# Kernel tuning notes

Measured on AMD Instinct MI355X. Metric: run time of the kernel, lower is better.

The kernel has to match this reference:

```python
import jax, jax.numpy as jnp
import numpy as np

N_NODES = 100000
N_EDGES = 3200000
N_FEAT = 64
HIDDEN = 20
N_CLASSES = 10
BN_EPS = 1e-5


def _lin_init(key, fan_in, fan_out):
    k1, k2 = jax.random.split(key)
    bound = 1.0 / np.sqrt(fan_in)
    W = jax.random.uniform(k1, (fan_in, fan_out), jnp.float32, -bound, bound)
    b = jax.random.uniform(k2, (fan_out,), jnp.float32, -bound, bound)
    return W, b


def setup_inputs() -> dict:
    key = jax.random.key(0)
    ks = jax.random.split(key, 12)
    x = jax.random.normal(ks[0], (N_NODES, N_FEAT), jnp.float32)
    edge_index = jax.random.randint(ks[1], (2, N_EDGES), 0, N_NODES, jnp.int32)
    edge_weights = jax.random.uniform(ks[2], (N_EDGES,), jnp.float32)
    w1a, b1a = _lin_init(ks[3], N_FEAT, HIDDEN)
    w2a, b2a = _lin_init(ks[4], HIDDEN, HIDDEN)
    w1b, b1b = _lin_init(ks[5], HIDDEN, HIDDEN)
    w2b, b2b = _lin_init(ks[6], HIDDEN, HIDDEN)
    w1c, b1c = _lin_init(ks[7], HIDDEN, HIDDEN)
    w2c, b2c = _lin_init(ks[8], HIDDEN, HIDDEN)
    wlin, blin = _lin_init(ks[9], 3 * HIDDEN, N_CLASSES)
    g1 = jnp.ones((HIDDEN,), jnp.float32); be1 = jnp.zeros((HIDDEN,), jnp.float32)
    g2 = jnp.ones((HIDDEN,), jnp.float32); be2 = jnp.zeros((HIDDEN,), jnp.float32)
    return {
        'x': x, 'edge_index': edge_index, 'edge_weights': edge_weights,
        'w1a': w1a, 'b1a': b1a, 'w2a': w2a, 'b2a': b2a, 'g1': g1, 'be1': be1,
        'w1b': w1b, 'b1b': b1b, 'w2b': w2b, 'b2b': b2b, 'g2': g2, 'be2': be2,
        'w1c': w1c, 'b1c': b1c, 'w2c': w2c, 'b2c': b2c,
        'wlin': wlin, 'blin': blin,
    }


def _gin_conv(h, src, dst, w, W1, b1, W2, b2):
    # gather source node features, scale per-edge, scatter-add at destination
    m = h[src] * w[:, None]                                  # [E, d]
    agg = jax.ops.segment_sum(m, dst, num_segments=N_NODES)  # [N, d]
    z = jax.nn.relu(agg @ W1 + b1)
    return jax.nn.relu(z @ W2 + b2)


def _bn(h, gamma, beta):
    mu = jnp.mean(h, axis=0)
    var = jnp.var(h, axis=0)
    return gamma * (h - mu) * jax.lax.rsqrt(var + BN_EPS) + beta


def reference(x, edge_index, edge_weights,
              w1a, b1a, w2a, b2a, g1, be1,
              w1b, b1b, w2b, b2b, g2, be2,
              w1c, b1c, w2c, b2c, wlin, blin):
    src, dst = edge_index[0], edge_index[1]
    o1 = _gin_conv(x, src, dst, edge_weights, w1a, b1a, w2a, b2a)
    o1 = _bn(jax.nn.relu(o1), g1, be1)
    o2 = _gin_conv(o1, src, dst, edge_weights, w1b, b1b, w2b, b2b)
    o2 = _bn(jax.nn.relu(o2), g2, be2)
    o3 = jax.nn.relu(_gin_conv(o2, src, dst, edge_weights, w1c, b1c, w2c, b2c))
    emb = jnp.concatenate([o1, o2, o3], axis=1)  # [N, 60]
    return emb @ wlin + blin
```

## Files before the change

kernel.cpp:

```cpp
#include <hip/hip_runtime.h>
#include <hip/hip_fp16.h>

#define N_NODES 100000
#define N_EDGES 3200000
#define N_FEAT  64
#define HIDDEN  20
#define N_CLASSES 10
#define BN_EPS  1e-5f
#define PNPB    51
#define GNPB    85
#define NREG    391
#define RCAP    10240
#define RCAP2   12288
#define TILE    4096
#define NTILE   ((N_EDGES + TILE - 1) / TILE)
#define EPT     16
#define WSCALE  (1.0f / 32767.0f)
#define YSTRIDE 24

__device__ __forceinline__ void fma8h(float4& lo, float4& hi, float s, const float4& raw) {
    const __half2* h = (const __half2*)&raw;
    float2 a = __half22float2(h[0]);
    float2 b = __half22float2(h[1]);
    float2 c = __half22float2(h[2]);
    float2 d = __half22float2(h[3]);
    lo.x += s * a.x; lo.y += s * a.y; lo.z += s * b.x; lo.w += s * b.y;
    hi.x += s * c.x; hi.y += s * c.y; hi.z += s * d.x; hi.w += s * d.y;
}

__global__ __launch_bounds__(256) void partition_kernel(const int* __restrict__ ei,
                                                        const float* __restrict__ ew,
                                                        int* __restrict__ rcur,
                                                        int2* __restrict__ staging) {
    __shared__ int hist[NREG];
    __shared__ int base[NREG];
    int tid = threadIdx.x;
    for (int r = tid; r < NREG; r += 256) hist[r] = 0;
    __syncthreads();

    int t0 = blockIdx.x * TILE;
    int2 ebuf[EPT];
    int  rbuf[EPT];
    #pragma unroll
    for (int k = 0; k < EPT; ++k) {
        int i = t0 + tid + k * 256;
        if (i < N_EDGES) {
            int src = ei[i];
            int dst = ei[N_EDGES + i];
            float w = ew[i];
            int r = dst >> 8;
            ebuf[k].x = src | ((dst & 255) << 17);
            ebuf[k].y = __float_as_int(w);
            rbuf[k] = r;
            atomicAdd(&hist[r], 1);
        } else {
            rbuf[k] = -1;
        }
    }
    __syncthreads();

    for (int r = tid; r < NREG; r += 256) {
        int c = hist[r];
        base[r] = (c > 0) ? atomicAdd(&rcur[r], c) : 0;
        hist[r] = 0;
    }
    __syncthreads();

    #pragma unroll
    for (int k = 0; k < EPT; ++k) {
        int r = rbuf[k];
        if (r >= 0) {
            int rank = atomicAdd(&hist[r], 1);
            int p = base[r] + rank;
            if (p < RCAP) staging[(size_t)r * RCAP + p] = ebuf[k];
        }
    }
}

__global__ __launch_bounds__(256) void region_kernel(const int* __restrict__ rcur,
                                                     const int2* __restrict__ staging,
                                                     int* __restrict__ rowstart,
                                                     int* __restrict__ nbatch,
                                                     int* __restrict__ edges) {
    __shared__ int h[256];
    __shared__ int s[256];
    int tid = threadIdx.x;
    int r = blockIdx.x;
    int cnt = min(rcur[r], RCAP);
    const int2* sg = staging + (size_t)r * RCAP;

    h[tid] = 0;
    __syncthreads();
    for (int i = tid; i < cnt; i += 256)
        atomicAdd(&h[(sg[i].x >> 17) & 255], 1);
    __syncthreads();

    int v = h[tid];
    int p = (v + 7) & ~7;
    s[tid] = p;
    __syncthreads();
    for (int off = 1; off < 256; off <<= 1) {
        int u = (tid >= off) ? s[tid - off] : 0;
        __syncthreads();
        s[tid] += u;
        __syncthreads();
    }
    int start = r * RCAP2 + (s[tid] - p);
    int node = (r << 8) + tid;
    if (node < N_NODES) {
        rowstart[node] = start;
        nbatch[node] = p >> 3;
    }
    h[tid] = start;
    __syncthreads();

    for (int i = tid; i < cnt; i += 256) {
        int2 e = sg[i];
        int dl = (e.x >> 17) & 255;
        int wq = __float2int_rn(__int_as_float(e.y) * 32767.0f);
        wq = min(max(wq, 0), 32767);
        int pos = atomicAdd(&h[dl], 1);
        edges[pos] = (e.x & 0x1FFFF) | (wq << 17);
    }
    __syncthreads();
    for (int jj = start + v; jj < start + p; ++jj) edges[jj] = 0;
}

__global__ __launch_bounds__(256) void pre1_kernel(const float* __restrict__ x,
                                                   const float* __restrict__ W1,
                                                   __half* __restrict__ y) {
    __shared__ float sW[N_FEAT * HIDDEN];
    __shared__ float sx[PNPB * 65];
    int tid = threadIdx.x;
    for (int i = tid; i < N_FEAT * HIDDEN; i += 256) sW[i] = W1[i];
    int base = blockIdx.x * PNPB;
    int nrows = min(PNPB, N_NODES - base);
    int total = nrows * N_FEAT;
    const float* xb = x + (size_t)base * N_FEAT;
    for (int i = tid; i < total; i += 256) {
        int r = i >> 6, c = i & 63;
        sx[r * 65 + c] = xb[i];
    }
    __syncthreads();

    int n_local = tid / 5;
    int q = tid - n_local * 5;
    int n = base + n_local;
    if (tid >= 255 || n >= N_NODES) return;

    float a0 = 0.f, a1 = 0.f, a2 = 0.f, a3 = 0.f;
    const float* row = &sx[n_local * 65];
    const float* wq = &sW[4 * q];
    #pragma unroll
    for (int k = 0; k < N_FEAT; ++k) {
        float xv = row[k];
        a0 += xv * wq[k * HIDDEN + 0];
        a1 += xv * wq[k * HIDDEN + 1];
        a2 += xv * wq[k * HIDDEN + 2];
        a3 += xv * wq[k * HIDDEN + 3];
    }
    if (q < 4) {
        float2 st;
        ((__half2*)&st)[0] = __floats2half2_rn(a0, a1);
        ((__half2*)&st)[1] = __floats2half2_rn(a2, a3);
        *(float2*)(y + (size_t)n * YSTRIDE + 4 * q) = st;
    } else {
        float4 st4;
        __half2* hp = (__half2*)&st4;
        hp[0] = __floats2half2_rn(a0, a1);
        hp[1] = __floats2half2_rn(a2, a3);
        hp[2] = __floats2half2_rn(0.f, 0.f);
        hp[3] = __floats2half2_rn(0.f, 0.f);
        *(float4*)(y + (size_t)n * YSTRIDE + 16) = st4;
    }
}

template <bool STATS, bool FINAL>
__global__ __launch_bounds__(512) void gin_fused(const int* __restrict__ rowstart,
                                                 const int* __restrict__ nbatch,
                                                 const int* __restrict__ edges,
                                                 const __half* __restrict__ y,
                                                 const float* __restrict__ b1,
                                                 const float* __restrict__ W2,
                                                 const float* __restrict__ b2,
                                                 float* __restrict__ opre,
                                                 float* __restrict__ stats,
                                                 const float* __restrict__ o1bn,
                                                 const float* __restrict__ o2bn,
                                                 const float* __restrict__ wlin,
                                                 const float* __restrict__ blin,
                                                 float* __restrict__ out) {
    __shared__ float pbuf[2 * GNPB * 24];
    __shared__ float zsh[GNPB * HIDDEN];
    __shared__ float sW2[HIDDEN * HIDDEN];
    __shared__ float sb1[HIDDEN];
    __shared__ float sb2[HIDDEN];
    __shared__ float sstat[STATS ? 2 * HIDDEN : 1];
    __shared__ float swl[FINAL ? (3 * HIDDEN * N_CLASSES + N_CLASSES) : 1];

    int tid = threadIdx.x;
    for (int i = tid; i < HIDDEN * HIDDEN; i += 512) sW2[i] = W2[i];
    if (tid < HIDDEN) { sb1[tid] = b1[tid]; sb2[tid] = b2[tid]; }
    if (STATS) {
        if (tid < 2 * HIDDEN) sstat[tid] = 0.f;
    }
    float* sw = swl;
    float* sb = swl + 3 * HIDDEN * N_CLASSES;
    if (FINAL) {
        for (int i = tid; i < 3 * HIDDEN * N_CLASSES; i += 512) sw[i] = wlin[i];
        if (tid < N_CLASSES) sb[tid] = blin[tid];
    }
    __syncthreads();

    {
        int n_local = tid / 6;
        int sub = tid - n_local * 6;
        int j = sub % 3;
        int g = sub / 3;
        int n = blockIdx.x * GNPB + n_local;
        bool act = (tid < 510) && (n < N_NODES);

        const __half* ybase = y + 8 * j;
        float4 a0l = make_float4(0.f, 0.f, 0.f, 0.f);
        float4 a0h = a0l, a1l = a0l, a1h = a0l;

        if (act) {
            int s0 = rowstart[n];
            int nb = nbatch[n];
            int bh = (nb + 1) >> 1;
            int b0 = g ? bh : 0;
            int b1e = g ? nb : bh;
            for (int b = b0; b < b1e; ++b) {
                const int* ep = edges + s0 + b * 8;
                int4 ea = *(const int4*)ep;
                int4 eb = *(const int4*)(ep + 4);
                float4 v0 = *(const float4*)(ybase + (size_t)(ea.x & 0x1FFFF) * YSTRIDE);
                float4 v1 = *(const float4*)(ybase + (size_t)(ea.y & 0x1FFFF) * YSTRIDE);
                float4 v2 = *(const float4*)(ybase + (size_t)(ea.z & 0x1FFFF) * YSTRIDE);
                float4 v3 = *(const float4*)(ybase + (size_t)(ea.w & 0x1FFFF) * YSTRIDE);
                float4 v4 = *(const float4*)(ybase + (size_t)(eb.x & 0x1FFFF) * YSTRIDE);
                float4 v5 = *(const float4*)(ybase + (size_t)(eb.y & 0x1FFFF) * YSTRIDE);
                float4 v6 = *(const float4*)(ybase + (size_t)(eb.z & 0x1FFFF) * YSTRIDE);
                float4 v7 = *(const float4*)(ybase + (size_t)(eb.w & 0x1FFFF) * YSTRIDE);
                fma8h(a0l, a0h, (float)((unsigned)ea.x >> 17) * WSCALE, v0);
                fma8h(a1l, a1h, (float)((unsigned)ea.y >> 17) * WSCALE, v1);
                fma8h(a0l, a0h, (float)((unsigned)ea.z >> 17) * WSCALE, v2);
                fma8h(a1l, a1h, (float)((unsigned)ea.w >> 17) * WSCALE, v3);
                fma8h(a0l, a0h, (float)((unsigned)eb.x >> 17) * WSCALE, v4);
                fma8h(a1l, a1h, (float)((unsigned)eb.y >> 17) * WSCALE, v5);
                fma8h(a0l, a0h, (float)((unsigned)eb.z >> 17) * WSCALE, v6);
                fma8h(a1l, a1h, (float)((unsigned)eb.w >> 17) * WSCALE, v7);
            }
        }
        a0l.x += a1l.x; a0l.y += a1l.y; a0l.z += a1l.z; a0l.w += a1l.w;
        a0h.x += a1h.x; a0h.y += a1h.y; a0h.z += a1h.z; a0h.w += a1h.w;

        if (act) {
            float* pr = &pbuf[(g * GNPB + n_local) * 24 + 8 * j];
            *(float4*)pr = a0l;
            *((float4*)pr + 1) = a0h;
        }
    }
    __syncthreads();

    int nl = tid / 5;
    int q = tid - nl * 5;
    int n = blockIdx.x * GNPB + nl;
    bool act5 = (tid < 5 * GNPB) && (n < N_NODES);

    if (act5) {
        const float* za = &pbuf[nl * 24];
        const float* zb = &pbuf[(GNPB + nl) * 24];
        float* zr = &zsh[nl * HIDDEN + 4 * q];
        #pragma unroll
        for (int i = 0; i < 4; ++i) {
            int f = 4 * q + i;
            zr[i] = fmaxf(za[f] + zb[f] + sb1[f], 0.f);
        }
    }
    __syncthreads();

    float o[4] = {0.f, 0.f, 0.f, 0.f};
    if (act5) {
        o[0] = sb2[4 * q + 0]; o[1] = sb2[4 * q + 1];
        o[2] = sb2[4 * q + 2]; o[3] = sb2[4 * q + 3];
        const float* zr = &zsh[nl * HIDDEN];
        const float* wq = &sW2[4 * q];
        #pragma unroll
        for (int k = 0; k < HIDDEN; ++k) {
            float zk = zr[k];
            o[0] += zk * wq[k * HIDDEN + 0];
            o[1] += zk * wq[k * HIDDEN + 1];
            o[2] += zk * wq[k * HIDDEN + 2];
            o[3] += zk * wq[k * HIDDEN + 3];
        }
        #pragma unroll
        for (int j2 = 0; j2 < 4; ++j2) o[j2] = fmaxf(o[j2], 0.f);
        if (!FINAL) {
            float* wr = opre + (size_t)n * HIDDEN + 4 * q;
            *(float4*)wr = make_float4(o[0], o[1], o[2], o[3]);
        }
    }

    if (STATS) {
        if (act5) {
            #pragma unroll
            for (int j2 = 0; j2 < 4; ++j2) {
                atomicAdd(&sstat[4 * q + j2], o[j2]);
                atomicAdd(&sstat[HIDDEN + 4 * q + j2], o[j2] * o[j2]);
            }
        }
        __syncthreads();
        if (tid < 2 * HIDDEN) atomicAdd(&stats[tid], sstat[tid]);
    }

    if (FINAL) {
        __syncthreads();
        float* osh1 = pbuf;
        float* osh2 = pbuf + GNPB * HIDDEN;
        if (act5) {
            float* zr = &zsh[nl * HIDDEN + 4 * q];
            zr[0] = o[0]; zr[1] = o[1]; zr[2] = o[2]; zr[3] = o[3];
            float4 v1 = *(const float4*)(o1bn + (size_t)n * HIDDEN + 4 * q);
            float4 v2 = *(const float4*)(o2bn + (size_t)n * HIDDEN + 4 * q);
            float* p1 = &osh1[nl * HIDDEN + 4 * q];
            float* p2 = &osh2[nl * HIDDEN + 4 * q];
            p1[0] = v1.x; p1[1] = v1.y; p1[2] = v1.z; p1[3] = v1.w;
            p2[0] = v2.x; p2[1] = v2.y; p2[2] = v2.z; p2[3] = v2.w;
        }
        __syncthreads();
        if (act5) {
            int c = 2 * q;
            float a0 = sb[c], a1 = sb[c + 1];
            const float* r1 = &osh1[nl * HIDDEN];
            const float* r2 = &osh2[nl * HIDDEN];
            const float* r3 = &zsh[nl * HIDDEN];
            #pragma unroll
            for (int j2 = 0; j2 < HIDDEN; ++j2) {
                float v = r1[j2];
                a0 += v * sw[j2 * N_CLASSES + c];
                a1 += v * sw[j2 * N_CLASSES + c + 1];
            }
            #pragma unroll
            for (int j2 = 0; j2 < HIDDEN; ++j2) {
                float v = r2[j2];
                a0 += v * sw[(HIDDEN + j2) * N_CLASSES + c];
                a1 += v * sw[(HIDDEN + j2) * N_CLASSES + c + 1];
            }
            #pragma unroll
            for (int j2 = 0; j2 < HIDDEN; ++j2) {
                float v = r3[j2];
                a0 += v * sw[(2 * HIDDEN + j2) * N_CLASSES + c];
                a1 += v * sw[(2 * HIDDEN + j2) * N_CLASSES + c + 1];
            }
            float* wr = out + (size_t)n * N_CLASSES + c;
            wr[0] = a0; wr[1] = a1;
        }
    }
}

__global__ __launch_bounds__(256) void bn_fuse(const float* __restrict__ opre,
                                               const float* __restrict__ stats,
                                               const float* __restrict__ gamma,
                                               const float* __restrict__ beta,
                                               float* __restrict__ obn,
                                               const float* __restrict__ Wnext,
                                               __half* __restrict__ y) {
    __shared__ float sc[HIDDEN], sh[HIDDEN];
    __shared__ float sW[HIDDEN * HIDDEN];
    __shared__ float hsh[PNPB * HIDDEN];
    int tid = threadIdx.x;
    for (int i = tid; i < HIDDEN * HIDDEN; i += 256) sW[i] = Wnext[i];
    if (tid < HIDDEN) {
        const float invN = 1.0f / N_NODES;
        float mu  = stats[tid] * invN;
        float var = stats[HIDDEN + tid] * invN - mu * mu;
        float inv = rsqrtf(var + BN_EPS);
        float s = gamma[tid] * inv;
        sc[tid] = s;
        sh[tid] = beta[tid] - mu * s;
    }
    __syncthreads();

    int n_local = tid / 5;
    int q = tid - n_local * 5;
    int n = blockIdx.x * PNPB + n_local;
    bool act = (tid < 255) && (n < N_NODES);

    if (act) {
        float4 v = *(const float4*)(opre + (size_t)n * HIDDEN + 4 * q);
        float h0 = v.x * sc[4 * q + 0] + sh[4 * q + 0];
        float h1 = v.y * sc[4 * q + 1] + sh[4 * q + 1];
        float h2 = v.z * sc[4 * q + 2] + sh[4 * q + 2];
        float h3 = v.w * sc[4 * q + 3] + sh[4 * q + 3];
        *(float4*)(obn + (size_t)n * HIDDEN + 4 * q) = make_float4(h0, h1, h2, h3);
        float* hr = &hsh[n_local * HIDDEN + 4 * q];
        hr[0] = h0; hr[1] = h1; hr[2] = h2; hr[3] = h3;
    }
    __syncthreads();

    if (act) {
        float a0 = 0.f, a1 = 0.f, a2 = 0.f, a3 = 0.f;
        const float* hr = &hsh[n_local * HIDDEN];
        const float* wq = &sW[4 * q];
        #pragma unroll
        for (int k = 0; k < HIDDEN; ++k) {
            float hk = hr[k];
            a0 += hk * wq[k * HIDDEN + 0];
            a1 += hk * wq[k * HIDDEN + 1];
            a2 += hk * wq[k * HIDDEN + 2];
            a3 += hk * wq[k * HIDDEN + 3];
        }
        float2 st;
        ((__half2*)&st)[0] = __floats2half2_rn(a0, a1);
        ((__half2*)&st)[1] = __floats2half2_rn(a2, a3);
        *(float2*)(y + (size_t)n * YSTRIDE + 4 * q) = st;
    }
}

extern "C" void kernel_launch(void* const* d_in, const int* in_sizes, int n_in,
                              void* d_out, int out_size, void* d_ws, size_t ws_size,
                              hipStream_t stream) {
    const float* x   = (const float*)d_in[0];
    const int*   ei  = (const int*)d_in[1];
    const float* ew  = (const float*)d_in[2];
    const float* w1a = (const float*)d_in[3];
    const float* b1a = (const float*)d_in[4];
    const float* w2a = (const float*)d_in[5];
    const float* b2a = (const float*)d_in[6];
    const float* g1  = (const float*)d_in[7];
    const float* be1 = (const float*)d_in[8];
    const float* w1b = (const float*)d_in[9];
    const float* b1b = (const float*)d_in[10];
    const float* w2b = (const float*)d_in[11];
    const float* b2b = (const float*)d_in[12];
    const float* g2  = (const float*)d_in[13];
    const float* be2 = (const float*)d_in[14];
    const float* w1c = (const float*)d_in[15];
    const float* b1c = (const float*)d_in[16];
    const float* w2c = (const float*)d_in[17];
    const float* b2c = (const float*)d_in[18];
    const float* wlin = (const float*)d_in[19];
    const float* blin = (const float*)d_in[20];
    float* out = (float*)d_out;

    char* base = (char*)d_ws;
    size_t ob = 0;
    int* rcur = (int*)(base + ob);      ob += NREG * 4;
    float* st1 = (float*)(base + ob);   ob += 2 * HIDDEN * 4;
    float* st2 = (float*)(base + ob);   ob += 2 * HIDDEN * 4;
    const size_t zero_bytes = ob;
    int* rowstart = (int*)(base + ob);  ob += N_NODES * 4;
    int* nbatch   = (int*)(base + ob);  ob += N_NODES * 4;
    ob = (ob + 63) & ~(size_t)63;
    int* edges = (int*)(base + ob);     ob += (size_t)NREG * RCAP2 * 4;
    ob = (ob + 63) & ~(size_t)63;
    const size_t u0 = ob;
    int2* staging = (int2*)(base + u0);
    __half* y   = (__half*)(base + u0);
    float* opre = (float*)(base + u0 + 4800000);
    float* o1bn = (float*)(base + u0 + 12800000);
    float* o2bn = (float*)(base + u0 + 20800000);

    const int preBlocks  = (N_NODES + PNPB - 1) / PNPB;
    const int gatBlocks  = (N_NODES + GNPB - 1) / GNPB;

    (void)hipMemsetAsync(base, 0, zero_bytes, stream);
    partition_kernel<<<NTILE, 256, 0, stream>>>(ei, ew, rcur, staging);
    region_kernel<<<NREG, 256, 0, stream>>>(rcur, staging, rowstart, nbatch, edges);

    pre1_kernel<<<preBlocks, 256, 0, stream>>>(x, w1a, y);
    gin_fused<true, false><<<gatBlocks, 512, 0, stream>>>(
        rowstart, nbatch, edges, y, b1a, w2a, b2a, opre, st1,
        o1bn, o2bn, wlin, blin, out);
    bn_fuse<<<preBlocks, 256, 0, stream>>>(opre, st1, g1, be1, o1bn, w1b, y);

    gin_fused<true, false><<<gatBlocks, 512, 0, stream>>>(
        rowstart, nbatch, edges, y, b1b, w2b, b2b, opre, st2,
        o1bn, o2bn, wlin, blin, out);
    bn_fuse<<<preBlocks, 256, 0, stream>>>(opre, st2, g2, be2, o2bn, w1c, y);

    gin_fused<false, true><<<gatBlocks, 512, 0, stream>>>(
        rowstart, nbatch, edges, y, b1c, w2c, b2c, opre, st1,
        o1bn, o2bn, wlin, blin, out);
}
```

Measured before the change: 260.7 us.

## Locally sort partition tile by region in shared memory for coalesced staging writes

The partition kernel now counts edges per region, computes a block-local prefix sum, scatters each edge into a region-sorted shared-memory buffer, and then writes to the global staging area in order of position. Consecutive threads therefore write consecutive slots within a region rather than scattered ones, which should coalesce better. Weight quantization moves from region_kernel into the partition kernel, and the region index is packed into the y field. In exchange the kernel uses 32KB of shared memory for the sorted tile plus extra scan barriers, which may lower occupancy.

```diff
diff --git a/kernel.cpp b/kernel.cpp
--- a/kernel.cpp
+++ b/kernel.cpp
@@ -32,47 +32,78 @@
                                                         const float* __restrict__ ew,
                                                         int* __restrict__ rcur,
                                                         int2* __restrict__ staging) {
-    __shared__ int hist[NREG];
-    __shared__ int base[NREG];
+    __shared__ int cnt[NREG];
+    __shared__ int lstart[NREG];
+    __shared__ int gbase[NREG];
+    __shared__ int cursor[NREG];
+    __shared__ int s2[256];
+    __shared__ int2 sorted[TILE];
     int tid = threadIdx.x;
-    for (int r = tid; r < NREG; r += 256) hist[r] = 0;
+    for (int r = tid; r < NREG; r += 256) cnt[r] = 0;
     __syncthreads();
 
     int t0 = blockIdx.x * TILE;
+    int tcnt = min(TILE, N_EDGES - t0);
     int2 ebuf[EPT];
-    int  rbuf[EPT];
     #pragma unroll
     for (int k = 0; k < EPT; ++k) {
         int i = t0 + tid + k * 256;
         if (i < N_EDGES) {
             int src = ei[i];
             int dst = ei[N_EDGES + i];
-            float w = ew[i];
+            int wq = __float2int_rn(ew[i] * 32767.0f);
+            wq = min(max(wq, 0), 32767);
             int r = dst >> 8;
             ebuf[k].x = src | ((dst & 255) << 17);
-            ebuf[k].y = __float_as_int(w);
-            rbuf[k] = r;
-            atomicAdd(&hist[r], 1);
+            ebuf[k].y = wq | (r << 15);
+            atomicAdd(&cnt[r], 1);
         } else {
-            rbuf[k] = -1;
-        }
-    }
+            ebuf[k].y = -1;
+        }
+    }
+    __syncthreads();
+
+    int a = (2 * tid < NREG) ? cnt[2 * tid] : 0;
+    int b = (2 * tid + 1 < NREG) ? cnt[2 * tid + 1] : 0;
+    s2[tid] = a + b;
+    __syncthreads();
+    for (int off = 1; off < 256; off <<= 1) {
+        int u = (tid >= off) ? s2[tid - off] : 0;
+        __syncthreads();
+        s2[tid] += u;
+        __syncthreads();
+    }
+    int ex = s2[tid] - (a + b);
+    if (2 * tid < NREG) lstart[2 * tid] = ex;
+    if (2 * tid + 1 < NREG) lstart[2 * tid + 1] = ex + a;
     __syncthreads();
 
     for (int r = tid; r < NREG; r += 256) {
-        int c = hist[r];
-        base[r] = (c > 0) ? atomicAdd(&rcur[r], c) : 0;
-        hist[r] = 0;
+        int c = cnt[r];
+        gbase[r] = (c > 0) ? atomicAdd(&rcur[r], c) : 0;
+        cursor[r] = lstart[r];
     }
     __syncthreads();
 
     #pragma unroll
     for (int k = 0; k < EPT; ++k) {
-        int r = rbuf[k];
-        if (r >= 0) {
-            int rank = atomicAdd(&hist[r], 1);
-            int p = base[r] + rank;
-            if (p < RCAP) staging[(size_t)r * RCAP + p] = ebuf[k];
+        if (ebuf[k].y >= 0) {
+            int r = ebuf[k].y >> 15;
+            int slot = atomicAdd(&cursor[r], 1);
+            sorted[slot] = ebuf[k];
+        }
+    }
+    __syncthreads();
+
+    for (int i = tid; i < tcnt; i += 256) {
+        int2 el = sorted[i];
+        int r = el.y >> 15;
+        int p = gbase[r] + (i - lstart[r]);
+        if (p < RCAP) {
+            int2 v;
+            v.x = el.x;
+            v.y = el.y & 0x7FFF;
+            staging[(size_t)r * RCAP + p] = v;
         }
     }
 }
@@ -117,10 +148,8 @@
     for (int i = tid; i < cnt; i += 256) {
         int2 e = sg[i];
         int dl = (e.x >> 17) & 255;
-        int wq = __float2int_rn(__int_as_float(e.y) * 32767.0f);
-        wq = min(max(wq, 0), 32767);
         int pos = atomicAdd(&h[dl], 1);
-        edges[pos] = (e.x & 0x1FFFF) | (wq << 17);
+        edges[pos] = (e.x & 0x1FFFF) | (e.y << 17);
     }
     __syncthreads();
     for (int jj = start + v; jj < start + p; ++jj) edges[jj] = 0;
```

Result: faster. 242.5 us (-7.0%).
